# Performance work log

Measured on AMD Instinct MI355X. Metric: run time of the kernel, lower is better.

Reference implementation:

```python
import jax, jax.numpy as jnp
import numpy as np

NOISE_WEIGHT = 1.0
CHAMFER_WEIGHT = 0.1
CHUNK = 1024


def _min_dist_chunked(a, b):
    """For each point in a [B,N,3], squared distance to nearest point in b [B,M,3].
    Processed in chunks of CHUNK points of `a` to avoid materializing [B,N,M].
    Returns [B,N]."""
    B, N, _ = a.shape
    b_sq = jnp.sum(b * b, axis=-1)  # [B,M]
    nc = N // CHUNK
    a_chunks = jnp.moveaxis(a.reshape(B, nc, CHUNK, 3), 1, 0)  # [nc,B,CHUNK,3]

    def body(carry, a_c):
        a_sq = jnp.sum(a_c * a_c, axis=-1)  # [B,CHUNK]
        # d[b,i,j] = |a_i|^2 + |b_j|^2 - 2 a_i.b_j
        d = a_sq[:, :, None] + b_sq[:, None, :] - 2.0 * jnp.einsum('bid,bjd->bij', a_c, b)
        d = jnp.maximum(d, 0.0)
        return carry, jnp.min(d, axis=2)  # [B,CHUNK]

    _, mins = jax.lax.scan(body, None, a_chunks)  # [nc,B,CHUNK]
    return jnp.moveaxis(mins, 0, 1).reshape(B, N)


def chamfer_distance(pred, target):
    d_pt = _min_dist_chunked(pred, target)   # [B,N]
    d_tp = _min_dist_chunked(target, pred)   # [B,M]
    return jnp.mean(d_pt, axis=1) + jnp.mean(d_tp, axis=1)  # [B]


def setup_inputs() -> dict:
    key = jax.random.key(0)
    k1, k2, k3, k4 = jax.random.split(key, 4)
    B, N = 8, 16384
    return {
        'predicted_noise': jax.random.normal(k1, (B, N, 3), dtype=jnp.float32),
        'actual_noise': jax.random.normal(k2, (B, N, 3), dtype=jnp.float32),
        'predicted_points_coarse': jax.random.normal(k3, (B, N, 3), dtype=jnp.float32),
        'target_points_coarse': jax.random.normal(k4, (B, N, 3), dtype=jnp.float32),
    }


def reference(predicted_noise, actual_noise, predicted_points_coarse, target_points_coarse):
    noise_loss = jnp.mean(jnp.abs(predicted_noise - actual_noise))
    chamfer_loss = jnp.mean(chamfer_distance(predicted_points_coarse, target_points_coarse))
    total_loss = NOISE_WEIGHT * noise_loss + CHAMFER_WEIGHT * chamfer_loss
    return total_loss
```

## Files before the change

kernel.cpp:

```cpp
#include <hip/hip_runtime.h>
#include <stdint.h>

#define NPTS        16384
#define BATCH       8
#define JC          512
#define NCHUNK      (NPTS / JC)
#define QPB         128
#define QBLKS       (NPTS / QPB)
#define CHAM_BLOCKS (BATCH * 2 * QBLKS)
#define NOISE_N     (BATCH * NPTS * 3)
#define NOISE_V4    (NOISE_N / 4)
#define NPTS_TOT    (BATCH * NPTS)
#define PACK_BLOCKS (NPTS_TOT / 256)

#define WS_NOISE_PART 0
#define WS_CHAM_PART  4096
#define WS_PK_PRED    16384
#define WS_PK_TARG    (WS_PK_PRED + 8 * NPTS_TOT)
#define WS_R_PRED     (WS_PK_TARG + 8 * NPTS_TOT)
#define WS_R_TARG     (WS_R_PRED + 4 * NPTS_TOT)

using halfx8 = __attribute__((ext_vector_type(8))) _Float16;
using f32x16 = __attribute__((ext_vector_type(16))) float;
using intx4  = __attribute__((ext_vector_type(4))) int;

__device__ __forceinline__ unsigned int f2h(float f) {
  union { _Float16 h; unsigned short s; } v; v.h = (_Float16)f; return v.s;
}
__device__ __forceinline__ float h2f(unsigned short s) {
  union { _Float16 h; unsigned short u; } v; v.u = s; return (float)v.h;
}
__device__ __forceinline__ float min3(float a, float b, float c) {
  return fminf(fminf(a, b), c);
}

__global__ void pack_noise_kernel(const float* __restrict__ pred,
                                  const float* __restrict__ targ,
                                  const float4* __restrict__ na,
                                  const float4* __restrict__ nb,
                                  ushort4* __restrict__ pk_pred,
                                  ushort4* __restrict__ pk_targ,
                                  float* __restrict__ r_pred,
                                  float* __restrict__ r_targ,
                                  float* __restrict__ part) {
  int i = blockIdx.x * 256 + threadIdx.x;
  {
    float x = pred[3*i+0], y = pred[3*i+1], z = pred[3*i+2];
    float s = __builtin_fmaf(x, x, __builtin_fmaf(y, y, z*z));
    pk_pred[i] = make_ushort4((unsigned short)f2h(x), (unsigned short)f2h(y),
                              (unsigned short)f2h(z), (unsigned short)f2h(s));
    r_pred[i] = s;
  }
  {
    float x = targ[3*i+0], y = targ[3*i+1], z = targ[3*i+2];
    float s = __builtin_fmaf(x, x, __builtin_fmaf(y, y, z*z));
    pk_targ[i] = make_ushort4((unsigned short)f2h(x), (unsigned short)f2h(y),
                              (unsigned short)f2h(z), (unsigned short)f2h(s));
    r_targ[i] = s;
  }
  float sn = 0.f;
  if (i < NOISE_V4) {
    float4 pa = na[i], pb = nb[i];
    sn = fabsf(pa.x-pb.x) + fabsf(pa.y-pb.y) + fabsf(pa.z-pb.z) + fabsf(pa.w-pb.w);
  }
  for (int o = 1; o < 64; o <<= 1) sn += __shfl_xor(sn, o);
  __shared__ float ws4[4];
  int lane = threadIdx.x & 63, wv = threadIdx.x >> 6;
  if (lane == 0) ws4[wv] = sn;
  __syncthreads();
  if (threadIdx.x == 0) part[blockIdx.x] = ws4[0] + ws4[1] + ws4[2] + ws4[3];
}

__global__ __launch_bounds__(256, 4)
void chamfer_kernel(const ushort4* __restrict__ pk_pred,
                    const ushort4* __restrict__ pk_targ,
                    const float* __restrict__ r_pred,
                    const float* __restrict__ r_targ,
                    float* __restrict__ part) {
  __shared__ __align__(16) ushort4 buf[2][JC];
  __shared__ float wsum[4];

  const int tid  = threadIdx.x;
  const int lane = tid & 63;
  const int wv   = tid >> 6;
  const int col  = lane & 31;

  const int blk  = blockIdx.x;
  const int qblk = blk & (QBLKS - 1);
  const int bd   = blk >> 7;
  const int dir  = bd & 1;
  const int b    = bd >> 1;

  const ushort4* qpk = dir ? pk_targ : pk_pred;
  const float*   qr  = dir ? r_targ  : r_pred;
  const ushort4* ref = dir ? pk_pred : pk_targ;
  qpk += b * NPTS; qr += b * NPTS; ref += b * NPTS;

  const int q = qblk * QPB + wv * 32 + col;
  ushort4 qt = qpk[q];
  unsigned int nx = f2h(-2.f * h2f(qt.x));
  unsigned int ny = f2h(-2.f * h2f(qt.y));
  unsigned int nz = f2h(-2.f * h2f(qt.z));
  unsigned int lo = (ny << 16) | nx;
  unsigned int hi = (0x3C00u << 16) | nz;
  const bool hh = (lane >= 32);

  union BF { halfx8 v; unsigned int u[4]; };
  BF fb0, fb1, fb2, fb3;
  fb0.u[0] = hh ? 0u : lo; fb0.u[1] = hh ? 0u : hi; fb0.u[2] = 0u;           fb0.u[3] = 0u;
  fb1.u[0] = 0u;           fb1.u[1] = 0u;           fb1.u[2] = hh ? 0u : lo; fb1.u[3] = hh ? 0u : hi;
  fb2.u[0] = hh ? lo : 0u; fb2.u[1] = hh ? hi : 0u; fb2.u[2] = 0u;           fb2.u[3] = 0u;
  fb3.u[0] = 0u;           fb3.u[1] = 0u;           fb3.u[2] = hh ? lo : 0u; fb3.u[3] = hh ? hi : 0u;

  f32x16 czero = {0.f,0.f,0.f,0.f, 0.f,0.f,0.f,0.f, 0.f,0.f,0.f,0.f, 0.f,0.f,0.f,0.f};

  auto stage = [&](int c, int pb) {
    const char* g = (const char*)ref + (size_t)c * (JC * 8) + wv * 1024 + lane * 16;
    char* l = (char*)&buf[pb][wv * 128];
    __builtin_amdgcn_global_load_lds(
        (const __attribute__((address_space(1))) unsigned int*)(uintptr_t)g,
        (__attribute__((address_space(3))) unsigned int*)(unsigned int)(uintptr_t)l,
        16, 0, 0);
  };

  stage(0, 0);

  union AF { intx4 i; halfx8 h; };

  float m = 1e30f;
  for (int c = 0; c < NCHUNK; ++c) {
    const int pp = c & 1;
    __syncthreads();
    if (c + 1 < NCHUNK) stage(c + 1, pp ^ 1);
    const char* base = (const char*)&buf[pp][0];
#pragma unroll
    for (int t = 0; t < 4; ++t) {
      AF fa;
      fa.i = *(const intx4*)(base + t * 1024 + lane * 16);
      f32x16 d0 = __builtin_amdgcn_mfma_f32_32x32x16_f16(fa.h, fb0.v, czero, 0, 0, 0);
      f32x16 d1 = __builtin_amdgcn_mfma_f32_32x32x16_f16(fa.h, fb1.v, czero, 0, 0, 0);
      f32x16 d2 = __builtin_amdgcn_mfma_f32_32x32x16_f16(fa.h, fb2.v, czero, 0, 0, 0);
      f32x16 d3 = __builtin_amdgcn_mfma_f32_32x32x16_f16(fa.h, fb3.v, czero, 0, 0, 0);
#pragma unroll
      for (int r = 0; r < 4; ++r) {
        const f32x16& d = (r == 0) ? d0 : (r == 1) ? d1 : (r == 2) ? d2 : d3;
        float t0 = min3(d[0],  d[1],  d[2]);
        float t1 = min3(d[3],  d[4],  d[5]);
        float t2 = min3(d[6],  d[7],  d[8]);
        float t3 = min3(d[9],  d[10], d[11]);
        float t4 = min3(d[12], d[13], d[14]);
        float u0 = min3(t0, t1, t2);
        float u1 = min3(t3, t4, d[15]);
        m = min3(m, u0, u1);
      }
    }
  }

  m = fminf(m, __shfl_xor(m, 32));
  float rq = qr[q];
  float dmin = fmaxf(rq + m, 0.f);
  float v = (lane < 32) ? dmin : 0.f;
  for (int o = 1; o < 32; o <<= 1) v += __shfl_xor(v, o);
  if (lane == 0) wsum[wv] = v;
  __syncthreads();
  if (tid == 0) part[blockIdx.x] = wsum[0] + wsum[1] + wsum[2] + wsum[3];
}

__global__ void final_kernel(const float* __restrict__ part_noise,
                             const float* __restrict__ part_cham,
                             float* __restrict__ out) {
  __shared__ float red[256];
  float s = 0.f;
  for (int i = threadIdx.x; i < PACK_BLOCKS; i += 256) s += part_noise[i];
  float t = 0.f;
  for (int i = threadIdx.x; i < CHAM_BLOCKS; i += 256) t += part_cham[i];
  red[threadIdx.x] = s; __syncthreads();
  for (int o = 128; o; o >>= 1) { if (threadIdx.x < o) red[threadIdx.x] += red[threadIdx.x + o]; __syncthreads(); }
  float noise_sum = red[0];
  __syncthreads();
  red[threadIdx.x] = t; __syncthreads();
  for (int o = 128; o; o >>= 1) { if (threadIdx.x < o) red[threadIdx.x] += red[threadIdx.x + o]; __syncthreads(); }
  if (threadIdx.x == 0)
    out[0] = noise_sum * (1.f / NOISE_N) + 0.1f * red[0] * (1.f / NPTS_TOT);
}

extern "C" void kernel_launch(void* const* d_in, const int* in_sizes, int n_in,
                              void* d_out, int out_size, void* d_ws, size_t ws_size,
                              hipStream_t stream) {
  const float* pn = (const float*)d_in[0];
  const float* an = (const float*)d_in[1];
  const float* pp = (const float*)d_in[2];
  const float* tp = (const float*)d_in[3];

  char* ws = (char*)d_ws;
  float*   noise_part = (float*)(ws + WS_NOISE_PART);
  float*   cham_part  = (float*)(ws + WS_CHAM_PART);
  ushort4* pk_pred    = (ushort4*)(ws + WS_PK_PRED);
  ushort4* pk_targ    = (ushort4*)(ws + WS_PK_TARG);
  float*   r_pred     = (float*)(ws + WS_R_PRED);
  float*   r_targ     = (float*)(ws + WS_R_TARG);

  pack_noise_kernel<<<PACK_BLOCKS, 256, 0, stream>>>(pp, tp, (const float4*)pn, (const float4*)an,
                                                     pk_pred, pk_targ, r_pred, r_targ, noise_part);
  chamfer_kernel<<<CHAM_BLOCKS, 256, 0, stream>>>(pk_pred, pk_targ, r_pred, r_targ, cham_part);
  final_kernel<<<1, 256, 0, stream>>>(noise_part, cham_part, (float*)d_out);
}
```

Measured before the change: 170.7 us.

## Shrink chamfer blocks to 128 threads, compute query norms inline, atomically reduce output

The chamfer kernel now runs 2 waves per block (64 queries) instead of 4. Each wave issues two LDS-direct loads per chunk stage. Query coordinates and squared norms are computed in fp32 from the raw inputs, so the r_pred/r_targ buffers are no longer needed. The final reduction kernel is replaced by a memset plus per-block atomicAdd into the output. These changes aim to improve occupancy and load balance and to drop one launch and some memory traffic, but twice as many blocks each reload the full reference set, and float atomics make the summation order nondeterministic.

```diff
diff --git a/kernel.cpp b/kernel.cpp
--- a/kernel.cpp
+++ b/kernel.cpp
@@ -5,7 +5,7 @@
 #define BATCH       8
 #define JC          512
 #define NCHUNK      (NPTS / JC)
-#define QPB         128
+#define QPB         64
 #define QBLKS       (NPTS / QPB)
 #define CHAM_BLOCKS (BATCH * 2 * QBLKS)
 #define NOISE_N     (BATCH * NPTS * 3)
@@ -13,12 +13,8 @@
 #define NPTS_TOT    (BATCH * NPTS)
 #define PACK_BLOCKS (NPTS_TOT / 256)
 
-#define WS_NOISE_PART 0
-#define WS_CHAM_PART  4096
-#define WS_PK_PRED    16384
-#define WS_PK_TARG    (WS_PK_PRED + 8 * NPTS_TOT)
-#define WS_R_PRED     (WS_PK_TARG + 8 * NPTS_TOT)
-#define WS_R_TARG     (WS_R_PRED + 4 * NPTS_TOT)
+#define WS_PK_PRED  0
+#define WS_PK_TARG  (8 * NPTS_TOT)
 
 using halfx8 = __attribute__((ext_vector_type(8))) _Float16;
 using f32x16 = __attribute__((ext_vector_type(16))) float;
@@ -27,11 +23,27 @@
 __device__ __forceinline__ unsigned int f2h(float f) {
   union { _Float16 h; unsigned short s; } v; v.h = (_Float16)f; return v.s;
 }
-__device__ __forceinline__ float h2f(unsigned short s) {
-  union { _Float16 h; unsigned short u; } v; v.u = s; return (float)v.h;
-}
 __device__ __forceinline__ float min3(float a, float b, float c) {
   return fminf(fminf(a, b), c);
+}
+
+__device__ __forceinline__ float red33(float m, const f32x16& A, const f32x16& B) {
+  float a0 = min3(A[0],  A[1],  A[2]);
+  float a1 = min3(A[3],  A[4],  A[5]);
+  float a2 = min3(A[6],  A[7],  A[8]);
+  float a3 = min3(A[9],  A[10], A[11]);
+  float a4 = min3(A[12], A[13], A[14]);
+  float b0 = min3(B[0],  B[1],  B[2]);
+  float b1 = min3(B[3],  B[4],  B[5]);
+  float b2 = min3(B[6],  B[7],  B[8]);
+  float b3 = min3(B[9],  B[10], B[11]);
+  float b4 = min3(B[12], B[13], B[14]);
+  float u0 = min3(a0, a1, a2);
+  float u1 = min3(a3, a4, A[15]);
+  float v0 = min3(b0, b1, b2);
+  float v1 = min3(b3, b4, B[15]);
+  float w0 = min3(u0, u1, v0);
+  return min3(m, w0, v1);
 }
 
 __global__ void pack_noise_kernel(const float* __restrict__ pred,
@@ -40,23 +52,19 @@
                                   const float4* __restrict__ nb,
                                   ushort4* __restrict__ pk_pred,
                                   ushort4* __restrict__ pk_targ,
-                                  float* __restrict__ r_pred,
-                                  float* __restrict__ r_targ,
-                                  float* __restrict__ part) {
+                                  float* __restrict__ out) {
   int i = blockIdx.x * 256 + threadIdx.x;
   {
     float x = pred[3*i+0], y = pred[3*i+1], z = pred[3*i+2];
     float s = __builtin_fmaf(x, x, __builtin_fmaf(y, y, z*z));
     pk_pred[i] = make_ushort4((unsigned short)f2h(x), (unsigned short)f2h(y),
                               (unsigned short)f2h(z), (unsigned short)f2h(s));
-    r_pred[i] = s;
   }
   {
     float x = targ[3*i+0], y = targ[3*i+1], z = targ[3*i+2];
     float s = __builtin_fmaf(x, x, __builtin_fmaf(y, y, z*z));
     pk_targ[i] = make_ushort4((unsigned short)f2h(x), (unsigned short)f2h(y),
                               (unsigned short)f2h(z), (unsigned short)f2h(s));
-    r_targ[i] = s;
   }
   float sn = 0.f;
   if (i < NOISE_V4) {
@@ -68,17 +76,18 @@
   int lane = threadIdx.x & 63, wv = threadIdx.x >> 6;
   if (lane == 0) ws4[wv] = sn;
   __syncthreads();
-  if (threadIdx.x == 0) part[blockIdx.x] = ws4[0] + ws4[1] + ws4[2] + ws4[3];
+  if (threadIdx.x == 0)
+    atomicAdd(out, (ws4[0] + ws4[1] + ws4[2] + ws4[3]) * (1.0f / NOISE_N));
 }
 
-__global__ __launch_bounds__(256, 4)
-void chamfer_kernel(const ushort4* __restrict__ pk_pred,
+__global__ __launch_bounds__(128, 6)
+void chamfer_kernel(const float* __restrict__ pred_f,
+                    const float* __restrict__ targ_f,
+                    const ushort4* __restrict__ pk_pred,
                     const ushort4* __restrict__ pk_targ,
-                    const float* __restrict__ r_pred,
-                    const float* __restrict__ r_targ,
-                    float* __restrict__ part) {
+                    float* __restrict__ out) {
   __shared__ __align__(16) ushort4 buf[2][JC];
-  __shared__ float wsum[4];
+  __shared__ float wsum[2];
 
   const int tid  = threadIdx.x;
   const int lane = tid & 63;
@@ -87,22 +96,19 @@
 
   const int blk  = blockIdx.x;
   const int qblk = blk & (QBLKS - 1);
-  const int bd   = blk >> 7;
+  const int bd   = blk >> 8;
   const int dir  = bd & 1;
   const int b    = bd >> 1;
 
-  const ushort4* qpk = dir ? pk_targ : pk_pred;
-  const float*   qr  = dir ? r_targ  : r_pred;
+  const float*   qf  = dir ? targ_f  : pred_f;
   const ushort4* ref = dir ? pk_pred : pk_targ;
-  qpk += b * NPTS; qr += b * NPTS; ref += b * NPTS;
+  qf += (size_t)b * NPTS * 3; ref += (size_t)b * NPTS;
 
-  const int q = qblk * QPB + wv * 32 + col;
-  ushort4 qt = qpk[q];
-  unsigned int nx = f2h(-2.f * h2f(qt.x));
-  unsigned int ny = f2h(-2.f * h2f(qt.y));
-  unsigned int nz = f2h(-2.f * h2f(qt.z));
-  unsigned int lo = (ny << 16) | nx;
-  unsigned int hi = (0x3C00u << 16) | nz;
+  const int qg = qblk * QPB + wv * 32 + col;
+  float qx = qf[3*qg+0], qy = qf[3*qg+1], qz = qf[3*qg+2];
+  float rq = __builtin_fmaf(qx, qx, __builtin_fmaf(qy, qy, qz*qz));
+  unsigned int lo = (f2h(-2.f*qy) << 16) | f2h(-2.f*qx);
+  unsigned int hi = (0x3C00u << 16) | f2h(-2.f*qz);
   const bool hh = (lane >= 32);
 
   union BF { halfx8 v; unsigned int u[4]; };
@@ -115,11 +121,16 @@
   f32x16 czero = {0.f,0.f,0.f,0.f, 0.f,0.f,0.f,0.f, 0.f,0.f,0.f,0.f, 0.f,0.f,0.f,0.f};
 
   auto stage = [&](int c, int pb) {
-    const char* g = (const char*)ref + (size_t)c * (JC * 8) + wv * 1024 + lane * 16;
-    char* l = (char*)&buf[pb][wv * 128];
+    size_t go = (size_t)c * (JC * 8) + wv * 2048 + lane * 16;
+    const char* g0 = (const char*)ref + go;
+    char* l0 = (char*)&buf[pb][0] + wv * 2048 + lane * 16;
     __builtin_amdgcn_global_load_lds(
-        (const __attribute__((address_space(1))) unsigned int*)(uintptr_t)g,
-        (__attribute__((address_space(3))) unsigned int*)(unsigned int)(uintptr_t)l,
+        (const __attribute__((address_space(1))) unsigned int*)(uintptr_t)g0,
+        (__attribute__((address_space(3))) unsigned int*)(unsigned int)(uintptr_t)l0,
+        16, 0, 0);
+    __builtin_amdgcn_global_load_lds(
+        (const __attribute__((address_space(1))) unsigned int*)(uintptr_t)(g0 + 1024),
+        (__attribute__((address_space(3))) unsigned int*)(unsigned int)(uintptr_t)(l0 + 1024),
         16, 0, 0);
   };
 
@@ -139,49 +150,21 @@
       fa.i = *(const intx4*)(base + t * 1024 + lane * 16);
       f32x16 d0 = __builtin_amdgcn_mfma_f32_32x32x16_f16(fa.h, fb0.v, czero, 0, 0, 0);
       f32x16 d1 = __builtin_amdgcn_mfma_f32_32x32x16_f16(fa.h, fb1.v, czero, 0, 0, 0);
+      m = red33(m, d0, d1);
       f32x16 d2 = __builtin_amdgcn_mfma_f32_32x32x16_f16(fa.h, fb2.v, czero, 0, 0, 0);
       f32x16 d3 = __builtin_amdgcn_mfma_f32_32x32x16_f16(fa.h, fb3.v, czero, 0, 0, 0);
-#pragma unroll
-      for (int r = 0; r < 4; ++r) {
-        const f32x16& d = (r == 0) ? d0 : (r == 1) ? d1 : (r == 2) ? d2 : d3;
-        float t0 = min3(d[0],  d[1],  d[2]);
-        float t1 = min3(d[3],  d[4],  d[5]);
-        float t2 = min3(d[6],  d[7],  d[8]);
-        float t3 = min3(d[9],  d[10], d[11]);
-        float t4 = min3(d[12], d[13], d[14]);
-        float u0 = min3(t0, t1, t2);
-        float u1 = min3(t3, t4, d[15]);
-        m = min3(m, u0, u1);
-      }
+      m = red33(m, d2, d3);
     }
   }
 
   m = fminf(m, __shfl_xor(m, 32));
-  float rq = qr[q];
   float dmin = fmaxf(rq + m, 0.f);
   float v = (lane < 32) ? dmin : 0.f;
   for (int o = 1; o < 32; o <<= 1) v += __shfl_xor(v, o);
   if (lane == 0) wsum[wv] = v;
   __syncthreads();
-  if (tid == 0) part[blockIdx.x] = wsum[0] + wsum[1] + wsum[2] + wsum[3];
-}
-
-__global__ void final_kernel(const float* __restrict__ part_noise,
-                             const float* __restrict__ part_cham,
-                             float* __restrict__ out) {
-  __shared__ float red[256];
-  float s = 0.f;
-  for (int i = threadIdx.x; i < PACK_BLOCKS; i += 256) s += part_noise[i];
-  float t = 0.f;
-  for (int i = threadIdx.x; i < CHAM_BLOCKS; i += 256) t += part_cham[i];
-  red[threadIdx.x] = s; __syncthreads();
-  for (int o = 128; o; o >>= 1) { if (threadIdx.x < o) red[threadIdx.x] += red[threadIdx.x + o]; __syncthreads(); }
-  float noise_sum = red[0];
-  __syncthreads();
-  red[threadIdx.x] = t; __syncthreads();
-  for (int o = 128; o; o >>= 1) { if (threadIdx.x < o) red[threadIdx.x] += red[threadIdx.x + o]; __syncthreads(); }
-  if (threadIdx.x == 0)
-    out[0] = noise_sum * (1.f / NOISE_N) + 0.1f * red[0] * (1.f / NPTS_TOT);
+  if (tid == 0)
+    atomicAdd(out, (wsum[0] + wsum[1]) * (0.1f / (float)NPTS_TOT));
 }
 
 extern "C" void kernel_launch(void* const* d_in, const int* in_sizes, int n_in,
@@ -193,15 +176,12 @@
   const float* tp = (const float*)d_in[3];
 
   char* ws = (char*)d_ws;
-  float*   noise_part = (float*)(ws + WS_NOISE_PART);
-  float*   cham_part  = (float*)(ws + WS_CHAM_PART);
-  ushort4* pk_pred    = (ushort4*)(ws + WS_PK_PRED);
-  ushort4* pk_targ    = (ushort4*)(ws + WS_PK_TARG);
-  float*   r_pred     = (float*)(ws + WS_R_PRED);
-  float*   r_targ     = (float*)(ws + WS_R_TARG);
+  ushort4* pk_pred = (ushort4*)(ws + WS_PK_PRED);
+  ushort4* pk_targ = (ushort4*)(ws + WS_PK_TARG);
+  float*   out     = (float*)d_out;
 
-  pack_noise_kernel<<<PACK_BLOCKS, 256, 0, stream>>>(pp, tp, (const float4*)pn, (const float4*)an,
-                                                     pk_pred, pk_targ, r_pred, r_targ, noise_part);
-  chamfer_kernel<<<CHAM_BLOCKS, 256, 0, stream>>>(pk_pred, pk_targ, r_pred, r_targ, cham_part);
-  final_kernel<<<1, 256, 0, stream>>>(noise_part, cham_part, (float*)d_out);
+  hipMemsetAsync(d_out, 0, sizeof(float), stream);
+  pack_noise_kernel<<<PACK_BLOCKS, 256, 0, stream>>>(pp, tp, (const float4*)pn,
+                                                     (const float4*)an, pk_pred, pk_targ, out);
+  chamfer_kernel<<<CHAM_BLOCKS, 128, 0, stream>>>(pp, tp, pk_pred, pk_targ, out);
 }
```

Result: slower. 181.0 us (+6.0%).
